# Kernel optimization log

Measured on AMD Instinct MI355X. Metric: run time of the kernel, lower is better.

Reference implementation:

```python
import jax, jax.numpy as jnp
import numpy as np
from jax import lax

B, T, D, H, W, K, E = 2, 16, 128, 64, 64, 3, 4


def setup_inputs() -> dict:
    key = jax.random.key(0)
    ks = jax.random.split(key, 20)

    def rn(k, shape, s):
        return (jax.random.normal(k, shape) * s).astype(jnp.float32)

    D2 = 2 * D
    inp = {
        "x_re": jax.random.normal(ks[0], (B, T, D, H, W), jnp.float32),
        "x_im": jax.random.normal(ks[1], (B, T, D, H, W), jnp.float32),
        # keep dt in [0.1, 1.0] (physical timestep, avoids sqrt(0) in noise term)
        "dt": (jax.random.uniform(ks[2], (B, T)) * 0.9 + 0.1).astype(jnp.float32),
        "ln_s_g": jnp.ones((D2,), jnp.float32),
        "ln_s_b": jnp.zeros((D2,), jnp.float32),
        "ln_t_g": jnp.ones((D2,), jnp.float32),
        "ln_t_b": jnp.zeros((D2,), jnp.float32),
        "conv_metric": (1.0 + 0.02 * jax.random.normal(ks[3], (D2, H, W))).astype(jnp.float32),
        "conv_w": rn(ks[4], (D2, D2, K, K), 1.0 / np.sqrt(D2 * K * K)),
        "conv_b": jnp.zeros((D2,), jnp.float32),
        "nu": rn(ks[5], (D,), 0.5),
        "theta": rn(ks[6], (D,), 1.0),
        "enc_re": rn(ks[7], (D, D), 1.0 / np.sqrt(D)),
        "enc_im": rn(ks[8], (D, D), 1.0 / np.sqrt(D)),
        "dec_re": rn(ks[9], (D, D), 1.0 / np.sqrt(D)),
        "dec_im": rn(ks[10], (D, D), 1.0 / np.sqrt(D)),
        "src_gain": rn(ks[11], (D,), 0.1),
        "w1_re": rn(ks[12], (D, E * D), 1.0 / np.sqrt(D)),
        "w1_im": rn(ks[13], (D, E * D), 1.0 / np.sqrt(D)),
        "b1_re": jnp.zeros((E * D,), jnp.float32),
        "b1_im": jnp.zeros((E * D,), jnp.float32),
        "w2_re": rn(ks[14], (E * D, D), 1.0 / np.sqrt(E * D)),
        "w2_im": rn(ks[15], (E * D, D), 1.0 / np.sqrt(E * D)),
        "b2_re": jnp.zeros((D,), jnp.float32),
        "b2_im": jnp.zeros((D,), jnp.float32),
    }
    return inp


def _ln(x, g, b):
    m = jnp.mean(x, -1, keepdims=True)
    v = jnp.var(x, -1, keepdims=True)
    return (x - m) * lax.rsqrt(v + 1e-5) * g + b


def _cnorm(z, g, b):
    # complex LayerNorm: LN over concat(real, imag) along last dim, then re-pack
    zn = _ln(jnp.concatenate([z.real, z.imag], -1), g, b)
    r, i = jnp.split(zn, 2, -1)
    return lax.complex(r, i)


def _forward(x_re, x_im, dt, ln_s_g, ln_s_b, ln_t_g, ln_t_b, conv_metric, conv_w, conv_b,
             nu, theta, enc_re, enc_im, dec_re, dec_im, src_gain,
             w1_re, w1_im, b1_re, b1_im, w2_re, w2_im, b2_re, b2_im):
    x = lax.complex(x_re, x_im)  # [B,T,D,H,W] complex64
    Bb, Tt, Dd, Hh, Ww = x.shape
    resid = x
    # ---- spatial branch: complex LN + metric-scaled (Riemannian) Clifford conv ----
    xs = jnp.transpose(x.reshape(Bb * Tt, Dd, Hh, Ww), (0, 2, 3, 1))  # [BT,H,W,D]
    xs = jnp.transpose(_cnorm(xs, ln_s_g, ln_s_b), (0, 3, 1, 2))      # [BT,D,H,W]
    xri = jnp.concatenate([xs.real, xs.imag], 1) * conv_metric[None]  # [BT,2D,H,W]
    pad = K // 2
    oc = lax.conv_general_dilated(xri, conv_w, (1, 1), ((pad, pad), (pad, pad)),
                                  dimension_numbers=("NCHW", "OIHW", "NCHW"))
    oc = oc + conv_b[None, :, None, None]
    r, i = jnp.split(oc, 2, 1)
    x = lax.complex(r, i).reshape(Bb, Tt, Dd, Hh, Ww) + resid
    resid = x
    # ---- temporal branch: eigen-encode, source law, ZOH forcing, parallel scan ----
    xt = jnp.transpose(x, (0, 3, 4, 1, 2)).reshape(Bb * Hh * Ww, Tt, Dd)  # [N,T,D]
    xt = _cnorm(xt, ln_t_g, ln_t_b)
    dte = jnp.broadcast_to(dt[:, None, None, :], (Bb, Hh, Ww, Tt)).reshape(Bb * Hh * Ww, Tt)
    lam = lax.complex(-jax.nn.softplus(nu), theta)                 # [D], Re<0 (stable)
    op_decay = jnp.exp(lam[None, None, :] * dte[:, :, None])       # [N,T,D] complex
    op_forcing = (op_decay - 1.0) / lam                            # zero-order hold
    xe = xt @ lax.complex(enc_re, enc_im)                          # eigenbasis encode
    src = lax.complex(jnp.tanh(xe.real), jnp.tanh(xe.imag)) * src_gain
    u = (xe + src) * op_forcing
    # stochastic term (fixed key -> deterministic reference)
    nk1, nk2 = jax.random.split(jax.random.key(42))
    amp = 0.01 * jnp.sqrt(dte)[:, :, None]
    u = u + lax.complex(amp * jax.random.normal(nk1, u.shape),
                        amp * jax.random.normal(nk2, u.shape))

    def comb(c1, c2):  # h_t = a_t * h_{t-1} + u_t
        a1, u1 = c1
        a2, u2 = c2
        return a1 * a2, a2 * u1 + u2

    _, h = lax.associative_scan(comb, (op_decay, u), axis=1)       # [N,T,D]
    xo = h @ lax.complex(dec_re, dec_im)                           # eigenbasis decode
    x_drift = jnp.transpose(xo.real.reshape(Bb, Hh, Ww, Tt, Dd), (0, 3, 4, 1, 2))
    x = x_drift + resid
    # ---- complex pointwise FFN ----
    z = jnp.transpose(x, (0, 1, 3, 4, 2))                          # [B,T,H,W,D]
    hdn = z @ lax.complex(w1_re, w1_im) + lax.complex(b1_re, b1_im)
    act = lax.complex(jax.nn.gelu(hdn.real), jax.nn.gelu(hdn.imag))
    delta = act @ lax.complex(w2_re, w2_im) + lax.complex(b2_re, b2_im)
    x = x + jnp.transpose(delta, (0, 1, 4, 2, 3))
    return jnp.stack([x.real, x.imag], -1)  # [B,T,D,H,W,2] float32


def reference(x_re, x_im, dt, ln_s_g, ln_s_b, ln_t_g, ln_t_b, conv_metric, conv_w, conv_b,
              nu, theta, enc_re, enc_im, dec_re, dec_im, src_gain,
              w1_re, w1_im, b1_re, b1_im, w2_re, w2_im, b2_re, b2_im):
    return _forward(x_re, x_im, dt, ln_s_g, ln_s_b, ln_t_g, ln_t_b, conv_metric, conv_w,
                    conv_b, nu, theta, enc_re, enc_im, dec_re, dec_im, src_gain,
                    w1_re, w1_im, b1_re, b1_im, w2_re, w2_im, b2_re, b2_im)
```

## Files before the change

### kernel.cpp

```cpp
#include <hip/hip_runtime.h>
#include <hip/hip_bf16.h>
#include <stdint.h>

#define B_   2
#define T_   16
#define D_   128
#define D2_  256
#define H_   64
#define W_   64
#define HW_  4096
#define BT_  32
#define N_   8192
#define ND_  1048576
#define PLANE_ 16777216
#define WT_FLOATS 589824

typedef short bf16x8 __attribute__((ext_vector_type(8)));
typedef float f32x4 __attribute__((ext_vector_type(4)));
typedef unsigned int uint;
typedef unsigned short ushort;


__device__ __forceinline__ float softplus_f(float x) {
  return fmaxf(x, 0.0f) + log1pf(expf(-fabsf(x)));
}

__device__ __forceinline__ float gelu_fast(float x) {
  const float Ac = 2.3022082963f;
  const float Bc = 0.1029437f;
  float t = x * x;
  float z = x * fmaf(Bc, t, Ac);
  float e = __builtin_amdgcn_exp2f(z);
  float r = __builtin_amdgcn_rcpf(e + 1.0f);
  return fmaf(-x, r, x);
}

__device__ __forceinline__ float tanh_fast(float x) {
  float e = __builtin_amdgcn_exp2f(x * 2.8853900818f);
  float r = __builtin_amdgcn_rcpf(e + 1.0f);
  return fmaf(-2.0f, r, 1.0f);
}

__device__ __forceinline__ ushort f2bf(float f) {
  uint u = __float_as_uint(f);
  uint r = (u + 0x7fffu + ((u >> 16) & 1u)) >> 16;
  return (ushort)r;
}

__device__ __forceinline__ uint cvt_pk(float a, float b) {
  __hip_bfloat162 h = __float22bfloat162_rn(make_float2(a, b));
  return *reinterpret_cast<uint*>(&h);
}


__global__ __launch_bounds__(256) void k_spatial_ln(
    const float* __restrict__ x_re, const float* __restrict__ x_im,
    const float* __restrict__ g, const float* __restrict__ bb,
    const float* __restrict__ metric, ushort* __restrict__ xri) {
  __shared__ float vals[256][64];
  __shared__ float red1[4][64];
  __shared__ float red2[4][64];
  __shared__ float mean_s[64];
  __shared__ float rstd_s[64];
  const int blk = blockIdx.x;
  const int bt = blk >> 6;
  const int h = blk & 63;
  const int tid = threadIdx.x;
  const int w = tid & 63, q = tid >> 6;

  const float* src = (q < 2) ? x_re : x_im;
  float s1 = 0.f, s2 = 0.f;
  #pragma unroll 4
  for (int i = 0; i < 64; ++i) {
    const int c = q * 64 + i;
    const int d = c & 127;
    float v = src[((size_t)bt * D_ + d) * HW_ + h * W_ + w];
    vals[c][w] = v;
    s1 += v; s2 += v * v;
  }
  red1[q][w] = s1; red2[q][w] = s2;
  __syncthreads();
  if (tid < 64) {
    float m = red1[0][tid] + red1[1][tid] + red1[2][tid] + red1[3][tid];
    float ss = red2[0][tid] + red2[1][tid] + red2[2][tid] + red2[3][tid];
    m *= (1.f / 256.f);
    float var = ss * (1.f / 256.f) - m * m;
    mean_s[tid] = m;
    rstd_s[tid] = rsqrtf(var + 1e-5f);
  }
  __syncthreads();
  const float m = mean_s[w], rs = rstd_s[w];
  const size_t ubase = (((size_t)bt * 64 + h) * 32 + q * 8) * 512 + w * 8;
  #pragma unroll
  for (int j = 0; j < 8; ++j) {
    uint4 u;
    #pragma unroll
    for (int e2 = 0; e2 < 4; ++e2) {
      const int c0 = q * 64 + j * 8 + e2 * 2;
      float v0 = (vals[c0][w] - m) * rs * g[c0] + bb[c0];
      v0 *= metric[(size_t)c0 * HW_ + h * W_ + w];
      float v1 = (vals[c0 + 1][w] - m) * rs * g[c0 + 1] + bb[c0 + 1];
      v1 *= metric[(size_t)(c0 + 1) * HW_ + h * W_ + w];
      ((uint*)&u)[e2] = cvt_pk(v0, v1);
    }
    *(uint4*)&xri[ubase + (size_t)j * 512] = u;
  }
}


__global__ __launch_bounds__(256) void k_prep_conv(
    const float* __restrict__ wg, ushort* __restrict__ cwswz) {
  const int t = blockIdx.x * 256 + threadIdx.x;
  if (t >= 73728) return;
  const int lane = t & 63;
  const int nt = (t >> 6) & 15;
  const int ks = (t >> 10) & 7;
  const int kk = t >> 13;
  const int co = nt * 16 + (lane & 15);
  const int ci0 = ks * 32 + (lane >> 4) * 8;
  ushort v[8];
  #pragma unroll
  for (int e = 0; e < 8; ++e)
    v[e] = f2bf(wg[((size_t)co * 256 + ci0 + e) * 9 + kk]);
  uint4 u;
  u.x = (uint)v[0] | ((uint)v[1] << 16);
  u.y = (uint)v[2] | ((uint)v[3] << 16);
  u.z = (uint)v[4] | ((uint)v[5] << 16);
  u.w = (uint)v[6] | ((uint)v[7] << 16);
  ((uint4*)cwswz)[t] = u;
}


__global__ __launch_bounds__(512, 4) void k_conv_mfma(
    const ushort* __restrict__ xri, const ushort* __restrict__ cwswz,
    const float* __restrict__ bias,
    const float* __restrict__ x_re, const float* __restrict__ x_im,
    float* __restrict__ x2_re, float* __restrict__ x2_im) {
  __shared__ ushort xb[33792];
  const int tid = threadIdx.x;
  const int wave = tid >> 6, lane = tid & 63;
  const int lrow = lane & 15, lgrp = lane >> 4;
  const int blk = blockIdx.x;
  const int bt = blk >> 5;
  const int h0 = (blk & 31) * 2;
  const int cw = wave & 3;
  const int sg = wave >> 2;

  f32x4 acc[4][4];
  #pragma unroll
  for (int j = 0; j < 4; ++j)
    #pragma unroll
    for (int i = 0; i < 4; ++i) acc[j][i] = (f32x4)0.f;

  for (int half = 0; half < 2; ++half) {
    __syncthreads();
    if (tid < 128) {
      const int j = tid >> 5;
      const int u = (tid >> 1) & 15;
      const int wz = (tid & 1) * 65;
      uint4 z = {0u, 0u, 0u, 0u};
      *(uint4*)&xb[((j * 16 + u) * 66 + wz) * 8] = z;
    }
    #pragma unroll
    for (int i = 0; i < 8; ++i) {
      const int idx = i * 512 + tid;
      const int w = idx & 63;
      const int u = (idx >> 6) & 15;
      const int j = idx >> 10;
      const int hh = h0 + j - 1;
      uint4 v = {0u, 0u, 0u, 0u};
      if (hh >= 0 && hh < 64)
        v = *(const uint4*)&xri[(((size_t)bt * 64 + hh) * 32 + half * 16 + u) * 512
                                + w * 8];
      *(uint4*)&xb[((j * 16 + u) * 66 + 1 + w) * 8] = v;
    }
    __syncthreads();

    for (int kh = 0; kh < 3; ++kh) {
      for (int kw = 0; kw < 3; ++kw) {
        const int kk = kh * 3 + kw;
        #pragma unroll
        for (int ks = 0; ks < 4; ++ks) {
          bf16x8 bfr[4];
          #pragma unroll
          for (int i = 0; i < 4; ++i)
            bfr[i] = *(const bf16x8*)&xb[(((sg + kh) * 16 + ks * 4 + lgrp) * 66
                                          + i * 16 + lrow + kw) * 8];
          const int fbase = ((kk * 8 + half * 4 + ks) * 16 + cw * 4) * 64 + lane;
          #pragma unroll
          for (int j = 0; j < 4; ++j) {
            const bf16x8 afr = ((const bf16x8*)cwswz)[fbase + j * 64];
            #pragma unroll
            for (int i = 0; i < 4; ++i)
              acc[j][i] = __builtin_amdgcn_mfma_f32_16x16x32_bf16(
                  afr, bfr[i], acc[j][i], 0, 0, 0);
          }
        }
      }
    }
  }

  #pragma unroll
  for (int j = 0; j < 4; ++j) {
    #pragma unroll
    for (int jj = 0; jj < 4; ++jj) {
      const int co = (cw * 4 + j) * 16 + lgrp * 4 + jj;
      const int d = co & 127;
      const float bv = bias[co];
      const float* rsrc = (co < 128) ? x_re : x_im;
      float* dst = (co < 128) ? x2_re : x2_im;
      const size_t rowoff = ((size_t)bt * D_ + d) * HW_ + (h0 + sg) * W_;
      #pragma unroll
      for (int i = 0; i < 4; ++i) {
        const int w = i * 16 + lrow;
        dst[rowoff + w] = acc[j][i][jj] + bv + rsrc[rowoff + w];
      }
    }
  }
}


__global__ __launch_bounds__(256) void k_prep_decay(
    const float* __restrict__ dt, const float* __restrict__ nu,
    const float* __restrict__ theta, float4* __restrict__ decay) {
  const int idx = blockIdx.x * 256 + threadIdx.x;
  const int d = idx & 127;
  const int bt = idx >> 7;
  const float dtv = dt[bt];
  const float lr = -softplus_f(nu[d]);
  const float li = theta[d];
  float s, c;
  sincosf(li * dtv, &s, &c);
  const float er = expf(lr * dtv);
  const float ar = er * c, ai = er * s;
  const float den = lr * lr + li * li;
  const float nr = ar - 1.f, ni = ai;
  float4 v;
  v.x = ar; v.y = ai;
  v.z = (nr * lr + ni * li) / den;
  v.w = (ni * lr - nr * li) / den;
  decay[idx] = v;
}


__global__ __launch_bounds__(256) void k_prep_enc(
    const float* __restrict__ enc_re, const float* __restrict__ enc_im,
    const float* __restrict__ g, ushort* __restrict__ encswz) {
  const int t = blockIdx.x * 256 + threadIdx.x;
  const int lane = t & 63;
  const int ks = (t >> 6) & 7;
  const int ntile = t >> 9;
  const int n = ntile * 16 + (lane & 15);
  const int k0 = ks * 32 + (lane >> 4) * 8;
  ushort v[8];
  #pragma unroll
  for (int e = 0; e < 8; ++e) {
    const int kp = k0 + e;
    const int k = (kp >> 1) | ((kp & 1) << 7);
    float val;
    if (k < 128) {
      val = (n < 128) ? enc_re[k * 128 + n] : enc_im[k * 128 + (n - 128)];
    } else {
      const int kk = k - 128;
      val = (n < 128) ? -enc_im[kk * 128 + n] : enc_re[kk * 128 + (n - 128)];
    }
    v[e] = f2bf(val * g[k]);
  }
  uint4 u;
  u.x = (uint)v[0] | ((uint)v[1] << 16);
  u.y = (uint)v[2] | ((uint)v[3] << 16);
  u.z = (uint)v[4] | ((uint)v[5] << 16);
  u.w = (uint)v[6] | ((uint)v[7] << 16);
  ((uint4*)encswz)[t] = u;
}

__global__ __launch_bounds__(256) void k_prep_encvec(
    const float* __restrict__ enc_re, const float* __restrict__ enc_im,
    const float* __restrict__ g, const float* __restrict__ bb,
    float* __restrict__ evec, float* __restrict__ cvec) {
  const int n = threadIdx.x;
  float se = 0.f, sc = 0.f;
  for (int k = 0; k < 256; ++k) {
    float ep;
    if (k < 128) {
      ep = (n < 128) ? enc_re[k * 128 + n] : enc_im[k * 128 + (n - 128)];
    } else {
      const int kk = k - 128;
      ep = (n < 128) ? -enc_im[kk * 128 + n] : enc_re[kk * 128 + (n - 128)];
    }
    se = fmaf(g[k], ep, se);
    sc = fmaf(bb[k], ep, sc);
  }
  evec[n] = se;
  cvec[n] = sc;
}

__global__ __launch_bounds__(256) void k_prep_dec(
    const float* __restrict__ dec_re, const float* __restrict__ dec_im,
    ushort* __restrict__ decswz) {
  const int t = blockIdx.x * 256 + threadIdx.x;
  const int lane = t & 63;
  const int ks = (t >> 6) & 7;
  const int ntile = t >> 9;
  const int n = ntile * 16 + (lane & 15);
  const int k0 = ks * 32 + (lane >> 4) * 8;
  ushort v[8];
  #pragma unroll
  for (int e = 0; e < 8; ++e) {
    const int kp = k0 + e;
    const int k = (kp >> 1) | ((kp & 1) << 7);
    float val = (k < 128) ? dec_re[k * 128 + n] : -dec_im[(k - 128) * 128 + n];
    v[e] = f2bf(val);
  }
  uint4 u;
  u.x = (uint)v[0] | ((uint)v[1] << 16);
  u.y = (uint)v[2] | ((uint)v[3] << 16);
  u.z = (uint)v[4] | ((uint)v[5] << 16);
  u.w = (uint)v[6] | ((uint)v[7] << 16);
  ((uint4*)decswz)[t] = u;
}


__global__ __launch_bounds__(256, 2) void k_temporal_mfma(
    const float* __restrict__ x2_re, const float* __restrict__ x2_im,
    const ushort* __restrict__ encswz,
    const float* __restrict__ evec, const float* __restrict__ cvec,
    const float4* __restrict__ decay,
    const float* __restrict__ src_gain,
    uint* __restrict__ u32) {
  __shared__ ushort xlds[64][256];
  __shared__ float red1[4][64], red2[4][64];
  __shared__ float mean_s[64], rstd_s[64];
  __shared__ float fre_s[128], fim_s[128], gain_s[128];
  const int tid = threadIdx.x;
  const int wave = tid >> 6, lane = tid & 63;
  const int lrow = lane & 15, lgrp = lane >> 4;
  const int blk = blockIdx.x;
  const int h = blk & 63;
  const int t = (blk >> 6) & 15;
  const int b = blk >> 10;
  const int bt = b * T_ + t;
  const size_t base = (size_t)bt * D_ * HW_ + h * W_;

  float s1 = 0.f, s2 = 0.f;
  #pragma unroll
  for (int i = 0; i < 8; ++i) {
    const int q = i * 4 + wave;
    const size_t g = base + (size_t)(q * 4) * HW_ + lane;
    float r0 = x2_re[g],           i0 = x2_im[g];
    float r1 = x2_re[g + HW_],     i1 = x2_im[g + HW_];
    float r2 = x2_re[g + 2 * HW_], i2 = x2_im[g + 2 * HW_];
    float r3 = x2_re[g + 3 * HW_], i3 = x2_im[g + 3 * HW_];
    uint4 u;
    u.x = cvt_pk(r0, i0); u.y = cvt_pk(r1, i1);
    u.z = cvt_pk(r2, i2); u.w = cvt_pk(r3, i3);
    *(uint4*)&xlds[lane][(q ^ (lane & 7)) << 3] = u;
    s1 += (r0 + r1 + r2 + r3) + (i0 + i1 + i2 + i3);
    s2 += r0 * r0 + r1 * r1 + r2 * r2 + r3 * r3
        + i0 * i0 + i1 * i1 + i2 * i2 + i3 * i3;
  }
  red1[wave][lane] = s1;
  red2[wave][lane] = s2;
  __syncthreads();
  if (tid < 64) {
    float m = red1[0][tid] + red1[1][tid] + red1[2][tid] + red1[3][tid];
    float ss = red2[0][tid] + red2[1][tid] + red2[2][tid] + red2[3][tid];
    m *= (1.f / 256.f);
    float var = ss * (1.f / 256.f) - m * m;
    mean_s[tid] = m;
    rstd_s[tid] = rsqrtf(var + 1e-5f);
  }
  if (tid < 128) {
    const float4 dc = decay[bt * 128 + tid];
    fre_s[tid] = dc.z;
    fim_s[tid] = dc.w;
    gain_s[tid] = src_gain[tid];
  }
  __syncthreads();

  f32x4 acc[4][4];
  #pragma unroll
  for (int ntl = 0; ntl < 4; ++ntl)
    #pragma unroll
    for (int st = 0; st < 4; ++st) acc[ntl][st] = (f32x4)0.f;

  const int swz = lrow & 7;
  const int ntb[4] = {wave * 2, wave * 2 + 1, wave * 2 + 8, wave * 2 + 9};
  #pragma unroll
  for (int ks = 0; ks < 8; ++ks) {
    bf16x8 bfr[4];
    #pragma unroll
    for (int st = 0; st < 4; ++st)
      bfr[st] = *(const bf16x8*)&xlds[st * 16 + lrow][(((ks * 4 + lgrp) ^ swz)) << 3];
    #pragma unroll
    for (int ntl = 0; ntl < 4; ++ntl) {
      const bf16x8 afr = ((const bf16x8*)encswz)[(ntb[ntl] * 8 + ks) * 64 + lane];
      #pragma unroll
      for (int st = 0; st < 4; ++st)
        acc[ntl][st] = __builtin_amdgcn_mfma_f32_16x16x32_bf16(
            afr, bfr[st], acc[ntl][st], 0, 0, 0);
    }
  }

  const int nbase = (b * 64 + h) * 64;
  #pragma unroll
  for (int ntl = 0; ntl < 2; ++ntl) {
    const int d0 = ntb[ntl] * 16 + lgrp * 4;
    #pragma unroll
    for (int st = 0; st < 4; ++st) {
      const int site = st * 16 + lrow;
      const float m = mean_s[site], rs = rstd_s[site];
      #pragma unroll
      for (int j = 0; j < 4; ++j) {
        const int d = d0 + j;
        const float xer = rs * acc[ntl][st][j] - rs * m * evec[d] + cvec[d];
        const float xei = rs * acc[ntl + 2][st][j] - rs * m * evec[d + 128] + cvec[d + 128];
        const float sr = tanh_fast(xer) * gain_s[d];
        const float si = tanh_fast(xei) * gain_s[d];
        const float vr = xer + sr, vi = xei + si;
        const float ur = vr * fre_s[d] - vi * fim_s[d];
        const float ui = vr * fim_s[d] + vi * fre_s[d];
        u32[(size_t)t * ND_ + (size_t)d * N_ + nbase + site] = cvt_pk(ur, ui);
      }
    }
  }
}


__global__ __launch_bounds__(256) void k_scan(
    uint* __restrict__ u32, const float4* __restrict__ decay) {
  const int idx = blockIdx.x * 256 + threadIdx.x;
  const int n = idx & 8191;
  const int d = idx >> 13;
  const int b = n >> 12;
  float hr = 0.f, hi = 0.f;
  #pragma unroll
  for (int t = 0; t < 16; ++t) {
    const float4 dc = decay[(b * 16 + t) * 128 + d];
    const size_t off = (size_t)t * ND_ + idx;
    const uint v = u32[off];
    const float ur = __uint_as_float(v << 16);
    const float ui = __uint_as_float(v & 0xffff0000u);
    const float nr = fmaf(dc.x, hr, fmaf(-dc.y, hi, ur));
    const float ni = fmaf(dc.x, hi, fmaf(dc.y, hr, ui));
    hr = nr; hi = ni;
    u32[off] = cvt_pk(hr, hi);
  }
}


__global__ __launch_bounds__(256, 2) void k_decode_mfma(
    const uint* __restrict__ h32, const ushort* __restrict__ decswz,
    float* __restrict__ x2_re) {
  __shared__ ushort xlds[64][256];
  const int tid = threadIdx.x;
  const int wave = tid >> 6, lane = tid & 63;
  const int lrow = lane & 15, lgrp = lane >> 4;
  const int blk = blockIdx.x;
  const int h = blk & 63;
  const int t = (blk >> 6) & 15;
  const int b = blk >> 10;
  const int bt = b * T_ + t;
  const int nbase = (b * 64 + h) * 64;

  #pragma unroll
  for (int i = 0; i < 8; ++i) {
    const int q = i * 4 + wave;
    const size_t o = (size_t)t * ND_ + (size_t)(q * 4) * N_ + nbase + lane;
    uint4 u;
    u.x = h32[o];
    u.y = h32[o + N_];
    u.z = h32[o + 2 * N_];
    u.w = h32[o + 3 * N_];
    *(uint4*)&xlds[lane][(q ^ (lane & 7)) << 3] = u;
  }
  __syncthreads();

  f32x4 acc[2][4];
  #pragma unroll
  for (int ntl = 0; ntl < 2; ++ntl)
    #pragma unroll
    for (int st = 0; st < 4; ++st) acc[ntl][st] = (f32x4)0.f;

  const int swz = lrow & 7;
  #pragma unroll
  for (int ks = 0; ks < 8; ++ks) {
    bf16x8 bfr[4];
    #pragma unroll
    for (int st = 0; st < 4; ++st)
      bfr[st] = *(const bf16x8*)&xlds[st * 16 + lrow][(((ks * 4 + lgrp) ^ swz)) << 3];
    #pragma unroll
    for (int ntl = 0; ntl < 2; ++ntl) {
      const int ntile = wave * 2 + ntl;
      const bf16x8 afr = ((const bf16x8*)decswz)[(ntile * 8 + ks) * 64 + lane];
      #pragma unroll
      for (int st = 0; st < 4; ++st)
        acc[ntl][st] = __builtin_amdgcn_mfma_f32_16x16x32_bf16(
            afr, bfr[st], acc[ntl][st], 0, 0, 0);
    }
  }

  #pragma unroll
  for (int ntl = 0; ntl < 2; ++ntl) {
    #pragma unroll
    for (int j = 0; j < 4; ++j) {
      const int d = (wave * 2 + ntl) * 16 + lgrp * 4 + j;
      const size_t rowoff = ((size_t)bt * D_ + d) * HW_ + h * W_;
      #pragma unroll
      for (int st = 0; st < 4; ++st) {
        const int site = st * 16 + lrow;
        x2_re[rowoff + site] += acc[ntl][st][j];
      }
    }
  }
}


__global__ __launch_bounds__(256) void k_prep_b1(
    const float* __restrict__ w1_re, const float* __restrict__ w1_im,
    ushort* __restrict__ b1swz) {
  const int t = blockIdx.x * 256 + threadIdx.x;
  const int lane = t & 63;
  const int ks = (t >> 6) & 7;
  const int ntile = t >> 9;
  const int n = ntile * 16 + (lane & 15);
  const int k0 = ks * 32 + (lane >> 4) * 8;
  ushort v[8];
  #pragma unroll
  for (int e = 0; e < 8; ++e) {
    const int kp = k0 + e;
    const int k = (kp >> 1) | ((kp & 1) << 7);
    float val;
    if (k < 128) {
      val = (n < 512) ? w1_re[k * 512 + n] : w1_im[k * 512 + (n - 512)];
    } else {
      const int kk = k - 128;
      val = (n < 512) ? -w1_im[kk * 512 + n] : w1_re[kk * 512 + (n - 512)];
    }
    v[e] = f2bf(val);
  }
  uint4 u;
  u.x = (uint)v[0] | ((uint)v[1] << 16);
  u.y = (uint)v[2] | ((uint)v[3] << 16);
  u.z = (uint)v[4] | ((uint)v[5] << 16);
  u.w = (uint)v[6] | ((uint)v[7] << 16);
  ((uint4*)b1swz)[t] = u;
}

__global__ __launch_bounds__(256) void k_prep_b2(
    const float* __restrict__ w2_re, const float* __restrict__ w2_im,
    ushort* __restrict__ b2swz) {
  const int t = blockIdx.x * 256 + threadIdx.x;
  const int lane = t & 63;
  const int kc = (t >> 6) & 31;
  const int rowtile = t >> 11;
  const int n2 = rowtile * 16 + (lane & 15);
  const int k0 = kc * 32 + (lane >> 4) * 8;
  ushort v[8];
  #pragma unroll
  for (int e = 0; e < 8; ++e) {
    const int k = k0 + e;
    float val;
    if (k < 512) {
      val = (n2 < 128) ? w2_re[k * 128 + n2] : w2_im[k * 128 + (n2 - 128)];
    } else {
      const int kk = k - 512;
      val = (n2 < 128) ? -w2_im[kk * 128 + n2] : w2_re[kk * 128 + (n2 - 128)];
    }
    v[e] = f2bf(val);
  }
  uint4 u;
  u.x = (uint)v[0] | ((uint)v[1] << 16);
  u.y = (uint)v[2] | ((uint)v[3] << 16);
  u.z = (uint)v[4] | ((uint)v[5] << 16);
  u.w = (uint)v[6] | ((uint)v[7] << 16);
  ((uint4*)b2swz)[t] = u;
}


__global__ __launch_bounds__(256, 2) void k_ffn_mfma(
    const float* __restrict__ x3_re, const float* __restrict__ x3_im,
    const ushort* __restrict__ b1swz, const ushort* __restrict__ b2swz,
    const float* __restrict__ b1_re, const float* __restrict__ b1_im,
    const float* __restrict__ b2_re, const float* __restrict__ b2_im,
    float* __restrict__ out) {
  __shared__ ushort xlds[64][256];
  __shared__ ushort actlds[2][64][136];
  const int tid = threadIdx.x;
  const int wave = tid >> 6, lane = tid & 63;
  const int lrow = lane & 15, lgrp = lane >> 4;
  const int blk = blockIdx.x;
  const int bt = blk >> 6;
  const int hw0 = (blk & 63) * 64;
  const size_t base = (size_t)bt * D_ * HW_ + hw0;
  const bf16x8* b1f = (const bf16x8*)b1swz;
  const bf16x8* b2f = (const bf16x8*)b2swz;

  #pragma unroll
  for (int i = 0; i < 8; ++i) {
    const int q = i * 4 + wave;
    const size_t g = base + (size_t)(q * 4) * HW_ + lane;
    uint4 u;
    u.x = cvt_pk(x3_re[g],           x3_im[g]);
    u.y = cvt_pk(x3_re[g + HW_],     x3_im[g + HW_]);
    u.z = cvt_pk(x3_re[g + 2 * HW_], x3_im[g + 2 * HW_]);
    u.w = cvt_pk(x3_re[g + 3 * HW_], x3_im[g + 3 * HW_]);
    *(uint4*)&xlds[lane][(q ^ (lane & 7)) << 3] = u;
  }

  bf16x8 a1[2][8];
  #pragma unroll
  for (int ntl = 0; ntl < 2; ++ntl)
    #pragma unroll
    for (int ks = 0; ks < 8; ++ks)
      a1[ntl][ks] = b1f[((wave * 2 + ntl) * 8 + ks) * 64 + lane];
  bf16x8 a2[4][2];
  #pragma unroll
  for (int rt = 0; rt < 4; ++rt)
    #pragma unroll
    for (int k2 = 0; k2 < 2; ++k2)
      a2[rt][k2] = b2f[((wave * 4 + rt) * 32 + k2) * 64 + lane];

  __syncthreads();

  f32x4 dacc[4][4];
  #pragma unroll
  for (int rt = 0; rt < 4; ++rt)
    #pragma unroll
    for (int st = 0; st < 4; ++st) dacc[rt][st] = (f32x4)0.f;

  const int swz = lrow & 7;

  for (int chunk = 0; chunk < 8; ++chunk) {
    const int nc = (chunk + 1) & 7;

    f32x4 hacc[2][4];
    #pragma unroll
    for (int ntl = 0; ntl < 2; ++ntl)
      #pragma unroll
      for (int st = 0; st < 4; ++st) hacc[ntl][st] = (f32x4)0.f;

    #pragma unroll
    for (int ks = 0; ks < 8; ++ks) {
      bf16x8 bfr[4];
      #pragma unroll
      for (int st = 0; st < 4; ++st)
        bfr[st] = *(const bf16x8*)&xlds[st * 16 + lrow][(((ks * 4 + lgrp) ^ swz)) << 3];
      #pragma unroll
      for (int ntl = 0; ntl < 2; ++ntl)
        #pragma unroll
        for (int st = 0; st < 4; ++st)
          hacc[ntl][st] = __builtin_amdgcn_mfma_f32_16x16x32_bf16(
              a1[ntl][ks], bfr[st], hacc[ntl][st], 0, 0, 0);
    }

    #pragma unroll
    for (int ntl = 0; ntl < 2; ++ntl)
      #pragma unroll
      for (int ks = 0; ks < 8; ++ks)
        a1[ntl][ks] = b1f[((nc * 8 + wave * 2 + ntl) * 8 + ks) * 64 + lane];

    uint* act32 = (uint*)&actlds[chunk & 1][0][0];
    #pragma unroll
    for (int ntl = 0; ntl < 2; ++ntl) {
      const int nlocal0 = (wave * 2 + ntl) * 16 + lgrp * 4;
      const int ng0 = chunk * 128 + nlocal0;
      #pragma unroll
      for (int st = 0; st < 4; ++st) {
        float gv[4];
        #pragma unroll
        for (int j = 0; j < 4; ++j) {
          const int ng = ng0 + j;
          const float bias = (ng < 512) ? b1_re[ng] : b1_im[ng - 512];
          gv[j] = gelu_fast(hacc[ntl][st][j] + bias);
        }
        const int site = st * 16 + lrow;
        act32[site * 68 + (nlocal0 >> 1)] = cvt_pk(gv[0], gv[1]);
        act32[site * 68 + (nlocal0 >> 1) + 1] = cvt_pk(gv[2], gv[3]);
      }
    }

    bf16x8 a2b[4][2];
    #pragma unroll
    for (int rt = 0; rt < 4; ++rt)
      #pragma unroll
      for (int k2 = 0; k2 < 2; ++k2)
        a2b[rt][k2] = b2f[((wave * 4 + rt) * 32 + chunk * 4 + 2 + k2) * 64 + lane];

    __syncthreads();

    const ushort* actb = &actlds[chunk & 1][0][0];
    #pragma unroll
    for (int ks2 = 0; ks2 < 2; ++ks2) {
      bf16x8 bfr[4];
      #pragma unroll
      for (int st = 0; st < 4; ++st)
        bfr[st] = *(const bf16x8*)&actb[(st * 16 + lrow) * 136 + ks2 * 32 + lgrp * 8];
      #pragma unroll
      for (int rt = 0; rt < 4; ++rt)
        #pragma unroll
        for (int st = 0; st < 4; ++st)
          dacc[rt][st] = __builtin_amdgcn_mfma_f32_16x16x32_bf16(
              a2[rt][ks2], bfr[st], dacc[rt][st], 0, 0, 0);
    }
    #pragma unroll
    for (int ks2 = 0; ks2 < 2; ++ks2) {
      bf16x8 bfr[4];
      #pragma unroll
      for (int st = 0; st < 4; ++st)
        bfr[st] = *(const bf16x8*)&actb[(st * 16 + lrow) * 136 + (ks2 + 2) * 32 + lgrp * 8];
      #pragma unroll
      for (int rt = 0; rt < 4; ++rt)
        #pragma unroll
        for (int st = 0; st < 4; ++st)
          dacc[rt][st] = __builtin_amdgcn_mfma_f32_16x16x32_bf16(
              a2b[rt][ks2], bfr[st], dacc[rt][st], 0, 0, 0);
    }

    #pragma unroll
    for (int rt = 0; rt < 4; ++rt)
      #pragma unroll
      for (int k2 = 0; k2 < 2; ++k2)
        a2[rt][k2] = b2f[((wave * 4 + rt) * 32 + nc * 4 + k2) * 64 + lane];
  }

  #pragma unroll
  for (int rt = 0; rt < 4; ++rt) {
    #pragma unroll
    for (int j = 0; j < 4; ++j) {
      const int n2 = (wave * 4 + rt) * 16 + lgrp * 4 + j;
      const int d = n2 & 127;
      const int c = n2 >> 7;
      const float bias2 = c ? b2_im[d] : b2_re[d];
      #pragma unroll
      for (int st = 0; st < 4; ++st) {
        const int site = st * 16 + lrow;
        const uint pr = *(const uint*)&xlds[site][(((d >> 2) ^ (site & 7)) << 3)
                                                  + (d & 3) * 2];
        const float rv = c ? __uint_as_float(pr & 0xffff0000u)
                           : __uint_as_float(pr << 16);
        const size_t idx = (size_t)(bt * D_ + d) * HW_ + hw0 + site;
        out[idx * 2 + c] = rv + dacc[rt][st][j] + bias2;
      }
    }
  }
}


extern "C" void kernel_launch(void* const* d_in, const int* in_sizes, int n_in,
                              void* d_out, int out_size, void* d_ws, size_t ws_size,
                              hipStream_t stream) {
  const float* x_re   = (const float*)d_in[0];
  const float* x_im   = (const float*)d_in[1];
  const float* dt     = (const float*)d_in[2];
  const float* ln_s_g = (const float*)d_in[3];
  const float* ln_s_b = (const float*)d_in[4];
  const float* ln_t_g = (const float*)d_in[5];
  const float* ln_t_b = (const float*)d_in[6];
  const float* metric = (const float*)d_in[7];
  const float* conv_w = (const float*)d_in[8];
  const float* conv_b = (const float*)d_in[9];
  const float* nu     = (const float*)d_in[10];
  const float* theta  = (const float*)d_in[11];
  const float* enc_re = (const float*)d_in[12];
  const float* enc_im = (const float*)d_in[13];
  const float* dec_re = (const float*)d_in[14];
  const float* dec_im = (const float*)d_in[15];
  const float* src_g  = (const float*)d_in[16];
  const float* w1_re  = (const float*)d_in[17];
  const float* w1_im  = (const float*)d_in[18];
  const float* b1_re  = (const float*)d_in[19];
  const float* b1_im  = (const float*)d_in[20];
  const float* w2_re  = (const float*)d_in[21];
  const float* w2_im  = (const float*)d_in[22];
  const float* b2_re  = (const float*)d_in[23];
  const float* b2_im  = (const float*)d_in[24];
  float* out = (float*)d_out;
  float* ws = (float*)d_ws;

  float* wt   = ws;
  float* bufA = ws + WT_FLOATS;
  ushort* wt16  = (ushort*)wt;
  ushort* cwswz = wt16;
  ushort* b1swz = wt16;
  ushort* b2swz = wt16 + 262144;
  ushort* encswz = wt16 + 524288;
  ushort* decswz = wt16 + 589824;
  float*  evec   = (float*)(wt16 + 622592);
  float*  cvec   = evec + 256;
  float4* decay  = (float4*)(cvec + 256);
  ushort* xri_bf = (ushort*)bufA;
  uint*   u32    = (uint*)bufA;

  const size_t needA = (size_t)(WT_FLOATS + 2 * PLANE_ + 2 * PLANE_) * 4;
  const bool planA = ws_size >= needA;
  float *x2_re, *x2_im, *ffn_out;
  if (planA) {
    x2_re = bufA + 2 * (size_t)PLANE_;
    x2_im = x2_re + PLANE_;
    ffn_out = out;
  } else {
    x2_re = out;
    x2_im = out + PLANE_;
    ffn_out = bufA;
  }

  k_prep_conv<<<288, 256, 0, stream>>>(conv_w, cwswz);
  k_prep_decay<<<16, 256, 0, stream>>>(dt, nu, theta, decay);
  k_spatial_ln<<<BT_ * H_, 256, 0, stream>>>(x_re, x_im, ln_s_g, ln_s_b, metric, xri_bf);
  k_conv_mfma<<<BT_ * 32, 512, 0, stream>>>(xri_bf, cwswz, conv_b, x_re, x_im,
                                            x2_re, x2_im);
  k_prep_b1<<<128, 256, 0, stream>>>(w1_re, w1_im, b1swz);
  k_prep_b2<<<128, 256, 0, stream>>>(w2_re, w2_im, b2swz);
  k_prep_enc<<<32, 256, 0, stream>>>(enc_re, enc_im, ln_t_g, encswz);
  k_prep_encvec<<<1, 256, 0, stream>>>(enc_re, enc_im, ln_t_g, ln_t_b, evec, cvec);
  k_prep_dec<<<16, 256, 0, stream>>>(dec_re, dec_im, decswz);
  k_temporal_mfma<<<B_ * T_ * H_, 256, 0, stream>>>(x2_re, x2_im, encswz,
                                                    evec, cvec, decay, src_g, u32);
  k_scan<<<ND_ / 256, 256, 0, stream>>>(u32, decay);
  k_decode_mfma<<<B_ * T_ * H_, 256, 0, stream>>>(u32, decswz, x2_re);
  k_ffn_mfma<<<BT_ * H_, 256, 0, stream>>>(x2_re, x2_im, b1swz, b2swz,
                                           b1_re, b1_im, b2_re, b2_im, ffn_out);
  if (!planA) {
    hipMemcpyAsync(d_out, ffn_out, (size_t)2 * PLANE_ * sizeof(float),
                   hipMemcpyDeviceToDevice, stream);
  }
}
```

Measured before the change: 694.1 us.

## Store conv output as packed bf16 pairs and fuse eigenbasis decode into FFN

```diff
diff --git a/kernel.cpp b/kernel.cpp
--- a/kernel.cpp
+++ b/kernel.cpp
@@ -135,7 +135,7 @@
     const ushort* __restrict__ xri, const ushort* __restrict__ cwswz,
     const float* __restrict__ bias,
     const float* __restrict__ x_re, const float* __restrict__ x_im,
-    float* __restrict__ x2_re, float* __restrict__ x2_im) {
+    uint* __restrict__ x2p) {
   __shared__ ushort xb[33792];
   const int tid = threadIdx.x;
   const int wave = tid >> 6, lane = tid & 63;
@@ -200,20 +200,41 @@
     }
   }
 
-  #pragma unroll
-  for (int j = 0; j < 4; ++j) {
-    #pragma unroll
-    for (int jj = 0; jj < 4; ++jj) {
-      const int co = (cw * 4 + j) * 16 + lgrp * 4 + jj;
-      const int d = co & 127;
-      const float bv = bias[co];
-      const float* rsrc = (co < 128) ? x_re : x_im;
-      float* dst = (co < 128) ? x2_re : x2_im;
-      const size_t rowoff = ((size_t)bt * D_ + d) * HW_ + (h0 + sg) * W_;
-      #pragma unroll
-      for (int i = 0; i < 4; ++i) {
-        const int w = i * 16 + lrow;
-        dst[rowoff + w] = acc[j][i][jj] + bv + rsrc[rowoff + w];
+  __syncthreads();
+  if (cw >= 2) {
+    #pragma unroll
+    for (int j = 0; j < 4; ++j) {
+      #pragma unroll
+      for (int jj = 0; jj < 4; ++jj) {
+        const int co = (cw * 4 + j) * 16 + lgrp * 4 + jj;
+        const int d = co - 128;
+        const float bv = bias[co];
+        const size_t rowoff = ((size_t)bt * D_ + d) * HW_ + (h0 + sg) * W_;
+        #pragma unroll
+        for (int i = 0; i < 4; ++i) {
+          const int w = i * 16 + lrow;
+          const float imv = acc[j][i][jj] + bv + x_im[rowoff + w];
+          xb[(sg * 64 + w) * 132 + d] = f2bf(imv);
+        }
+      }
+    }
+  }
+  __syncthreads();
+  if (cw < 2) {
+    #pragma unroll
+    for (int j = 0; j < 4; ++j) {
+      #pragma unroll
+      for (int jj = 0; jj < 4; ++jj) {
+        const int d = (cw * 4 + j) * 16 + lgrp * 4 + jj;
+        const float bv = bias[d];
+        const size_t rowoff = ((size_t)bt * D_ + d) * HW_ + (h0 + sg) * W_;
+        #pragma unroll
+        for (int i = 0; i < 4; ++i) {
+          const int w = i * 16 + lrow;
+          const float rev = acc[j][i][jj] + bv + x_re[rowoff + w];
+          const uint im16 = xb[(sg * 64 + w) * 132 + d];
+          x2p[rowoff + w] = (uint)f2bf(rev) | (im16 << 16);
+        }
       }
     }
   }
@@ -322,7 +343,7 @@
 
 
 __global__ __launch_bounds__(256, 2) void k_temporal_mfma(
-    const float* __restrict__ x2_re, const float* __restrict__ x2_im,
+    const uint* __restrict__ x2p,
     const ushort* __restrict__ encswz,
     const float* __restrict__ evec, const float* __restrict__ cvec,
     const float4* __restrict__ decay,
@@ -340,24 +361,26 @@
   const int t = (blk >> 6) & 15;
   const int b = blk >> 10;
   const int bt = b * T_ + t;
-  const size_t base = (size_t)bt * D_ * HW_ + h * W_;
 
   float s1 = 0.f, s2 = 0.f;
   #pragma unroll
   for (int i = 0; i < 8; ++i) {
     const int q = i * 4 + wave;
-    const size_t g = base + (size_t)(q * 4) * HW_ + lane;
-    float r0 = x2_re[g],           i0 = x2_im[g];
-    float r1 = x2_re[g + HW_],     i1 = x2_im[g + HW_];
-    float r2 = x2_re[g + 2 * HW_], i2 = x2_im[g + 2 * HW_];
-    float r3 = x2_re[g + 3 * HW_], i3 = x2_im[g + 3 * HW_];
+    const uint* src = &x2p[((size_t)bt * D_ + q * 4) * HW_ + h * W_ + lane];
     uint4 u;
-    u.x = cvt_pk(r0, i0); u.y = cvt_pk(r1, i1);
-    u.z = cvt_pk(r2, i2); u.w = cvt_pk(r3, i3);
+    u.x = src[0];
+    u.y = src[HW_];
+    u.z = src[2 * HW_];
+    u.w = src[3 * HW_];
     *(uint4*)&xlds[lane][(q ^ (lane & 7)) << 3] = u;
-    s1 += (r0 + r1 + r2 + r3) + (i0 + i1 + i2 + i3);
-    s2 += r0 * r0 + r1 * r1 + r2 * r2 + r3 * r3
-        + i0 * i0 + i1 * i1 + i2 * i2 + i3 * i3;
+    #pragma unroll
+    for (int e = 0; e < 4; ++e) {
+      const uint v = ((const uint*)&u)[e];
+      const float re = __uint_as_float(v << 16);
+      const float im = __uint_as_float(v & 0xffff0000u);
+      s1 += re + im;
+      s2 += re * re + im * im;
+    }
   }
   red1[wave][lane] = s1;
   red2[wave][lane] = s2;
@@ -449,73 +472,6 @@
 }
 
 
-__global__ __launch_bounds__(256, 2) void k_decode_mfma(
-    const uint* __restrict__ h32, const ushort* __restrict__ decswz,
-    float* __restrict__ x2_re) {
-  __shared__ ushort xlds[64][256];
-  const int tid = threadIdx.x;
-  const int wave = tid >> 6, lane = tid & 63;
-  const int lrow = lane & 15, lgrp = lane >> 4;
-  const int blk = blockIdx.x;
-  const int h = blk & 63;
-  const int t = (blk >> 6) & 15;
-  const int b = blk >> 10;
-  const int bt = b * T_ + t;
-  const int nbase = (b * 64 + h) * 64;
-
-  #pragma unroll
-  for (int i = 0; i < 8; ++i) {
-    const int q = i * 4 + wave;
-    const size_t o = (size_t)t * ND_ + (size_t)(q * 4) * N_ + nbase + lane;
-    uint4 u;
-    u.x = h32[o];
-    u.y = h32[o + N_];
-    u.z = h32[o + 2 * N_];
-    u.w = h32[o + 3 * N_];
-    *(uint4*)&xlds[lane][(q ^ (lane & 7)) << 3] = u;
-  }
-  __syncthreads();
-
-  f32x4 acc[2][4];
-  #pragma unroll
-  for (int ntl = 0; ntl < 2; ++ntl)
-    #pragma unroll
-    for (int st = 0; st < 4; ++st) acc[ntl][st] = (f32x4)0.f;
-
-  const int swz = lrow & 7;
-  #pragma unroll
-  for (int ks = 0; ks < 8; ++ks) {
-    bf16x8 bfr[4];
-    #pragma unroll
-    for (int st = 0; st < 4; ++st)
-      bfr[st] = *(const bf16x8*)&xlds[st * 16 + lrow][(((ks * 4 + lgrp) ^ swz)) << 3];
-    #pragma unroll
-    for (int ntl = 0; ntl < 2; ++ntl) {
-      const int ntile = wave * 2 + ntl;
-      const bf16x8 afr = ((const bf16x8*)decswz)[(ntile * 8 + ks) * 64 + lane];
-      #pragma unroll
-      for (int st = 0; st < 4; ++st)
-        acc[ntl][st] = __builtin_amdgcn_mfma_f32_16x16x32_bf16(
-            afr, bfr[st], acc[ntl][st], 0, 0, 0);
-    }
-  }
-
-  #pragma unroll
-  for (int ntl = 0; ntl < 2; ++ntl) {
-    #pragma unroll
-    for (int j = 0; j < 4; ++j) {
-      const int d = (wave * 2 + ntl) * 16 + lgrp * 4 + j;
-      const size_t rowoff = ((size_t)bt * D_ + d) * HW_ + h * W_;
-      #pragma unroll
-      for (int st = 0; st < 4; ++st) {
-        const int site = st * 16 + lrow;
-        x2_re[rowoff + site] += acc[ntl][st][j];
-      }
-    }
-  }
-}
-
-
 __global__ __launch_bounds__(256) void k_prep_b1(
     const float* __restrict__ w1_re, const float* __restrict__ w1_im,
     ushort* __restrict__ b1swz) {
@@ -579,7 +535,8 @@
 
 
 __global__ __launch_bounds__(256, 2) void k_ffn_mfma(
-    const float* __restrict__ x3_re, const float* __restrict__ x3_im,
+    const uint* __restrict__ x2p, const uint* __restrict__ h32,
+    const ushort* __restrict__ decswz,
     const ushort* __restrict__ b1swz, const ushort* __restrict__ b2swz,
     const float* __restrict__ b1_re, const float* __restrict__ b1_im,
     const float* __restrict__ b2_re, const float* __restrict__ b2_im,
@@ -591,21 +548,30 @@
   const int lrow = lane & 15, lgrp = lane >> 4;
   const int blk = blockIdx.x;
   const int bt = blk >> 6;
-  const int hw0 = (blk & 63) * 64;
-  const size_t base = (size_t)bt * D_ * HW_ + hw0;
+  const int hrow = blk & 63;
+  const int hw0 = hrow * 64;
+  const int b = bt >> 4, t = bt & 15;
+  const int nbase = (b * 64 + hrow) * 64;
   const bf16x8* b1f = (const bf16x8*)b1swz;
   const bf16x8* b2f = (const bf16x8*)b2swz;
+  const bf16x8* dcf = (const bf16x8*)decswz;
+  ushort* hbuf = &actlds[0][0][0];
 
   #pragma unroll
   for (int i = 0; i < 8; ++i) {
     const int q = i * 4 + wave;
-    const size_t g = base + (size_t)(q * 4) * HW_ + lane;
+    const uint* src = &x2p[((size_t)bt * D_ + q * 4) * HW_ + hw0 + lane];
     uint4 u;
-    u.x = cvt_pk(x3_re[g],           x3_im[g]);
-    u.y = cvt_pk(x3_re[g + HW_],     x3_im[g + HW_]);
-    u.z = cvt_pk(x3_re[g + 2 * HW_], x3_im[g + 2 * HW_]);
-    u.w = cvt_pk(x3_re[g + 3 * HW_], x3_im[g + 3 * HW_]);
+    u.x = src[0]; u.y = src[HW_]; u.z = src[2 * HW_]; u.w = src[3 * HW_];
     *(uint4*)&xlds[lane][(q ^ (lane & 7)) << 3] = u;
+  }
+  #pragma unroll
+  for (int i = 0; i < 8; ++i) {
+    const int q = i * 4 + wave;
+    const size_t o = (size_t)t * ND_ + (size_t)(q * 4) * N_ + nbase + lane;
+    uint4 u;
+    u.x = h32[o]; u.y = h32[o + N_]; u.z = h32[o + 2 * N_]; u.w = h32[o + 3 * N_];
+    *(uint4*)&hbuf[lane * 264 + ((q ^ (lane & 7)) << 3)] = u;
   }
 
   bf16x8 a1[2][8];
@@ -622,14 +588,53 @@
       a2[rt][k2] = b2f[((wave * 4 + rt) * 32 + k2) * 64 + lane];
 
   __syncthreads();
+  const int swz = lrow & 7;
+
+  {
+    f32x4 dr[2][4];
+    #pragma unroll
+    for (int ntl = 0; ntl < 2; ++ntl)
+      #pragma unroll
+      for (int st = 0; st < 4; ++st) dr[ntl][st] = (f32x4)0.f;
+    #pragma unroll
+    for (int ks = 0; ks < 8; ++ks) {
+      bf16x8 bfr[4];
+      #pragma unroll
+      for (int st = 0; st < 4; ++st)
+        bfr[st] = *(const bf16x8*)&hbuf[(st * 16 + lrow) * 264
+                                        + (((ks * 4 + lgrp) ^ swz) << 3)];
+      #pragma unroll
+      for (int ntl = 0; ntl < 2; ++ntl) {
+        const bf16x8 afr = dcf[((wave * 2 + ntl) * 8 + ks) * 64 + lane];
+        #pragma unroll
+        for (int st = 0; st < 4; ++st)
+          dr[ntl][st] = __builtin_amdgcn_mfma_f32_16x16x32_bf16(
+              afr, bfr[st], dr[ntl][st], 0, 0, 0);
+      }
+    }
+    #pragma unroll
+    for (int ntl = 0; ntl < 2; ++ntl) {
+      #pragma unroll
+      for (int st = 0; st < 4; ++st) {
+        const int site = st * 16 + lrow;
+        #pragma unroll
+        for (int j = 0; j < 4; ++j) {
+          const int d = (wave * 2 + ntl) * 16 + lgrp * 4 + j;
+          ushort* p = &xlds[site][(((d >> 2) ^ (site & 7)) << 3) + (d & 3) * 2];
+          const uint v = *(uint*)p;
+          const float re = __uint_as_float(v << 16) + dr[ntl][st][j];
+          *(uint*)p = (v & 0xffff0000u) | (uint)f2bf(re);
+        }
+      }
+    }
+  }
+  __syncthreads();
 
   f32x4 dacc[4][4];
   #pragma unroll
   for (int rt = 0; rt < 4; ++rt)
     #pragma unroll
     for (int st = 0; st < 4; ++st) dacc[rt][st] = (f32x4)0.f;
-
-  const int swz = lrow & 7;
 
   for (int chunk = 0; chunk < 8; ++chunk) {
     const int nc = (chunk + 1) & 7;
@@ -790,36 +795,34 @@
   float*  cvec   = evec + 256;
   float4* decay  = (float4*)(cvec + 256);
   ushort* xri_bf = (ushort*)bufA;
-  uint*   u32    = (uint*)bufA;
-
-  const size_t needA = (size_t)(WT_FLOATS + 2 * PLANE_ + 2 * PLANE_) * 4;
+
+  const size_t needA = ((size_t)WT_FLOATS + 2 * (size_t)PLANE_) * 4 + (1u << 20);
   const bool planA = ws_size >= needA;
-  float *x2_re, *x2_im, *ffn_out;
+  uint *u32p, *x2p;
+  float* ffn_out;
   if (planA) {
-    x2_re = bufA + 2 * (size_t)PLANE_;
-    x2_im = x2_re + PLANE_;
+    u32p = (uint*)bufA;
+    x2p  = (uint*)bufA + PLANE_;
     ffn_out = out;
   } else {
-    x2_re = out;
-    x2_im = out + PLANE_;
+    u32p = (uint*)out;
+    x2p  = (uint*)out + PLANE_;
     ffn_out = bufA;
   }
 
   k_prep_conv<<<288, 256, 0, stream>>>(conv_w, cwswz);
   k_prep_decay<<<16, 256, 0, stream>>>(dt, nu, theta, decay);
   k_spatial_ln<<<BT_ * H_, 256, 0, stream>>>(x_re, x_im, ln_s_g, ln_s_b, metric, xri_bf);
-  k_conv_mfma<<<BT_ * 32, 512, 0, stream>>>(xri_bf, cwswz, conv_b, x_re, x_im,
-                                            x2_re, x2_im);
+  k_conv_mfma<<<BT_ * 32, 512, 0, stream>>>(xri_bf, cwswz, conv_b, x_re, x_im, x2p);
   k_prep_b1<<<128, 256, 0, stream>>>(w1_re, w1_im, b1swz);
   k_prep_b2<<<128, 256, 0, stream>>>(w2_re, w2_im, b2swz);
   k_prep_enc<<<32, 256, 0, stream>>>(enc_re, enc_im, ln_t_g, encswz);
   k_prep_encvec<<<1, 256, 0, stream>>>(enc_re, enc_im, ln_t_g, ln_t_b, evec, cvec);
   k_prep_dec<<<16, 256, 0, stream>>>(dec_re, dec_im, decswz);
-  k_temporal_mfma<<<B_ * T_ * H_, 256, 0, stream>>>(x2_re, x2_im, encswz,
-                                                    evec, cvec, decay, src_g, u32);
-  k_scan<<<ND_ / 256, 256, 0, stream>>>(u32, decay);
-  k_decode_mfma<<<B_ * T_ * H_, 256, 0, stream>>>(u32, decswz, x2_re);
-  k_ffn_mfma<<<BT_ * H_, 256, 0, stream>>>(x2_re, x2_im, b1swz, b2swz,
+  k_temporal_mfma<<<B_ * T_ * H_, 256, 0, stream>>>(x2p, encswz, evec, cvec,
+                                                    decay, src_g, u32p);
+  k_scan<<<ND_ / 256, 256, 0, stream>>>(u32p, decay);
+  k_ffn_mfma<<<BT_ * H_, 256, 0, stream>>>(x2p, u32p, decswz, b1swz, b2swz,
                                            b1_re, b1_im, b2_re, b2_im, ffn_out);
   if (!planA) {
     hipMemcpyAsync(d_out, ffn_out, (size_t)2 * PLANE_ * sizeof(float),
```

New measurement: 664.8 us. 4.2% less time.
